# Kernel tuning notes

Measured on AMD Instinct MI355X. Metric: run time of the kernel, lower is better.

The kernel has to match this reference:

```python
import jax, jax.numpy as jnp
import numpy as np

MARGIN = 0.3  # from init_kwargs
N, D = 4096, 128


def _pairwise_sqdist(a, b):
    # ||a_i - b_j||^2 via the matmul identity; avoids an [N, N, D] intermediate.
    a2 = jnp.sum(a * a, axis=1)[:, None]
    b2 = jnp.sum(b * b, axis=1)[None, :]
    return a2 + b2 - 2.0 * (a @ b.T)


def setup_inputs() -> dict:
    key = jax.random.key(0)
    k1, k2 = jax.random.split(key)
    pair1 = jax.random.normal(k1, (N, D), dtype=jnp.float32)
    pair2 = jax.random.normal(k2, (N, D), dtype=jnp.float32)
    return {"pair1": pair1, "pair2": pair2}


def reference(pair1, pair2):
    n = pair1.shape[0]
    # positive distance per anchor: ||pair1[i] - pair2[i]||^2
    dist_ap = jnp.sum((pair1 - pair2) ** 2, axis=1)  # [N]
    D1 = _pairwise_sqdist(pair1, pair1)  # dist_an1[i, j]
    D2 = _pairwise_sqdist(pair1, pair2)  # dist_an2[i, j]
    L1 = jax.nn.relu(dist_ap[:, None] - D1 + MARGIN)  # [N, N]
    L2 = jax.nn.relu(dist_ap[:, None] - D2 + MARGIN)  # [N, N]
    # exclude j == i (the original `continue`); relu outputs are >= 0 and the
    # original hard-mining max starts at 0.0, so zeroing the diagonal is exact.
    offdiag = 1.0 - jnp.eye(n, dtype=L1.dtype)
    L1m = L1 * offdiag
    L2m = L2 * offdiag
    # online hard example mining: max loss per anchor over all 2*(N-1) negatives
    sub_loss = jnp.mean(jnp.maximum(jnp.max(L1m, axis=1), jnp.max(L2m, axis=1)))
    # average over all counted triplets: cnt = 2 * N * (N - 1)
    all_loss = (jnp.sum(L1m) + jnp.sum(L2m)) / (2.0 * n * (n - 1))
    return (sub_loss, all_loss)
```

## Files before the change

### kernel.cpp

```cpp
#include <hip/hip_runtime.h>
#include <hip/hip_bf16.h>

#define NN 4096
#define DD 128
#define MARGIN_F 0.3f
#define JC 128
#define GX (NN / JC)
#define GY (NN / 128)
#define NBLOCKS (GX * GY)
#define NT (JC / 16)

typedef __attribute__((ext_vector_type(8))) short bf16x8;
typedef __attribute__((ext_vector_type(4))) float f32x4;
typedef __attribute__((ext_vector_type(2))) float f32x2;


__device__ __forceinline__ ushort f2bf(float f) {
  __hip_bfloat16 h = __float2bfloat16(f);
  return *reinterpret_cast<ushort*>(&h);
}

__global__ __launch_bounds__(256) void ptl_prep(
    const float* __restrict__ p1, const float* __restrict__ p2,
    ushort* __restrict__ p1t, ushort* __restrict__ p2t,
    float* __restrict__ a2, float* __restrict__ b2, float* __restrict__ c,
    unsigned int* __restrict__ rowmax, float* __restrict__ sumacc,
    unsigned int* __restrict__ donecnt) {
  int row = blockIdx.x * 4 + (threadIdx.x >> 6);
  int lane = threadIdx.x & 63;
  float2 x = ((const float2*)(p1 + (size_t)row * DD))[lane];
  float2 y = ((const float2*)(p2 + (size_t)row * DD))[lane];
  ushort2 xb, yb;
  xb.x = f2bf(x.x); xb.y = f2bf(x.y);
  yb.x = f2bf(y.x); yb.y = f2bf(y.y);
  int k = lane * 2;
  size_t idx = (size_t)(row >> 4) * 2048 + (size_t)(k >> 5) * 512 +
               (size_t)((k & 31) >> 3) * 128 + (size_t)(row & 15) * 8 +
               (size_t)(k & 7);
  *(ushort2*)(p1t + idx) = xb;
  *(ushort2*)(p2t + idx) = yb;

  float sa = x.x * x.x + x.y * x.y;
  float sb = y.x * y.x + y.y * y.y;
  float d0 = x.x - y.x, d1 = x.y - y.y;
  float sd = d0 * d0 + d1 * d1;
#pragma unroll
  for (int off = 32; off > 0; off >>= 1) {
    sa += __shfl_down(sa, off);
    sb += __shfl_down(sb, off);
    sd += __shfl_down(sd, off);
  }
  if (lane == 0) {
    a2[row] = sa;
    b2[row] = sb;
    c[row] = sd - sa + MARGIN_F;
    rowmax[row] = 0u;
  }
  if (blockIdx.x == 0 && threadIdx.x == 0) {
    *sumacc = 0.f;
    *donecnt = 0u;
  }
}

__global__ __launch_bounds__(256) void ptl_mfma(
    const ushort* __restrict__ p1t, const ushort* __restrict__ p2t,
    const float* __restrict__ a2v, const float* __restrict__ b2v,
    const float* __restrict__ cvv, unsigned int* __restrict__ rowmax,
    float* __restrict__ sumacc, unsigned int* __restrict__ donecnt,
    float* __restrict__ out) {
  const int tid = threadIdx.x;
  const int w = tid >> 6;
  const int lane = tid & 63;
  const int col16 = lane & 15;
  const int quad = lane >> 4;
  const int rowBase = (blockIdx.y * 4 + w) * 32;
  const int jBase = blockIdx.x * JC;
  const int lofs = quad * 128 + col16 * 8;

  __shared__ float wsum[4];
  __shared__ float wm[4];
  __shared__ unsigned int ticket;

  bf16x8 afr[2][4];
#pragma unroll
  for (int st = 0; st < 2; ++st) {
    const ushort* pa = p1t + ((size_t)(rowBase >> 4) + st) * 2048 + lofs;
#pragma unroll
    for (int s = 0; s < 4; ++s) afr[st][s] = *(const bf16x8*)(pa + s * 512);
  }

  float cv[2][4];
#pragma unroll
  for (int st = 0; st < 2; ++st)
#pragma unroll
    for (int r = 0; r < 4; ++r) cv[st][r] = cvv[rowBase + st * 16 + quad * 4 + r];

  const ushort* pb1 = p1t + (size_t)(jBase >> 4) * 2048 + lofs;
  const ushort* pb2 = p2t + (size_t)(jBase >> 4) * 2048 + lofs;

  f32x2 lsum2 = {0.f, 0.f};
  f32x2 rmax2[2][4];
#pragma unroll
  for (int st = 0; st < 2; ++st)
#pragma unroll
    for (int r = 0; r < 4; ++r) rmax2[st][r] = (f32x2){0.f, 0.f};

#pragma unroll
  for (int jt = 0; jt < NT; ++jt) {
    bf16x8 b1[4], b2[4];
#pragma unroll
    for (int s = 0; s < 4; ++s) {
      b1[s] = *(const bf16x8*)(pb1 + (size_t)jt * 2048 + s * 512);
      b2[s] = *(const bf16x8*)(pb2 + (size_t)jt * 2048 + s * 512);
    }
    f32x4 acc[2][2];
#pragma unroll
    for (int st = 0; st < 2; ++st)
#pragma unroll
      for (int m = 0; m < 2; ++m) acc[st][m] = (f32x4){0.f, 0.f, 0.f, 0.f};
#pragma unroll
    for (int s = 0; s < 4; ++s) {
      acc[0][0] = __builtin_amdgcn_mfma_f32_16x16x32_bf16(afr[0][s], b1[s], acc[0][0], 0, 0, 0);
      acc[1][0] = __builtin_amdgcn_mfma_f32_16x16x32_bf16(afr[1][s], b1[s], acc[1][0], 0, 0, 0);
      acc[0][1] = __builtin_amdgcn_mfma_f32_16x16x32_bf16(afr[0][s], b2[s], acc[0][1], 0, 0, 0);
      acc[1][1] = __builtin_amdgcn_mfma_f32_16x16x32_bf16(afr[1][s], b2[s], acc[1][1], 0, 0, 0);
    }

    const int jcol = jBase + jt * 16 + col16;
    f32x2 nj = { a2v[jcol], b2v[jcol] };
#pragma unroll
    for (int st = 0; st < 2; ++st) {
      const bool diagT = (jBase + jt * 16) == (rowBase + st * 16);
#pragma unroll
      for (int r = 0; r < 4; ++r) {
        f32x2 t = { acc[st][0][r], acc[st][1][r] };
        f32x2 v = t * 2.f + (cv[st][r] - nj);
        v.x = fmaxf(v.x, 0.f);
        v.y = fmaxf(v.y, 0.f);
        if (diagT && col16 == quad * 4 + r) v = (f32x2){0.f, 0.f};
        lsum2 += v;
        rmax2[st][r].x = fmaxf(rmax2[st][r].x, v.x);
        rmax2[st][r].y = fmaxf(rmax2[st][r].y, v.y);
      }
    }
  }

  float lsum = lsum2.x + lsum2.y;
  float rmax[2][4];
#pragma unroll
  for (int st = 0; st < 2; ++st)
#pragma unroll
    for (int r = 0; r < 4; ++r)
      rmax[st][r] = fmaxf(rmax2[st][r].x, rmax2[st][r].y);

#pragma unroll
  for (int off = 8; off > 0; off >>= 1)
#pragma unroll
    for (int st = 0; st < 2; ++st)
#pragma unroll
      for (int r = 0; r < 4; ++r)
        rmax[st][r] = fmaxf(rmax[st][r], __shfl_xor(rmax[st][r], off));
  if (col16 == 0) {
#pragma unroll
    for (int st = 0; st < 2; ++st)
#pragma unroll
      for (int r = 0; r < 4; ++r)
        atomicMax(&rowmax[rowBase + st * 16 + quad * 4 + r],
                  __float_as_uint(rmax[st][r]));
  }

#pragma unroll
  for (int off = 32; off > 0; off >>= 1) lsum += __shfl_down(lsum, off);
  if (lane == 0) wsum[w] = lsum;
  __syncthreads();
  if (tid == 0) {
    atomicAdd(sumacc, wsum[0] + wsum[1] + wsum[2] + wsum[3]);
    __threadfence();
    ticket = atomicAdd(donecnt, 1u);
  }
  __syncthreads();

  if (ticket == NBLOCKS - 1) {
    __threadfence();
    float sm = 0.f;
#pragma unroll 4
    for (int i = tid; i < NN; i += 256)
      sm += __uint_as_float(atomicMax(&rowmax[i], 0u));
#pragma unroll
    for (int off = 32; off > 0; off >>= 1) sm += __shfl_down(sm, off);
    if (lane == 0) wm[w] = sm;
    __syncthreads();
    if (tid == 0) {
      float total = atomicAdd(sumacc, 0.f);
      out[0] = (wm[0] + wm[1] + wm[2] + wm[3]) / (float)NN;
      out[1] = total / (2.0f * (float)NN * (float)(NN - 1));
    }
  }
}

extern "C" void kernel_launch(void* const* d_in, const int* in_sizes, int n_in,
                              void* d_out, int out_size, void* d_ws, size_t ws_size,
                              hipStream_t stream) {
  const float* p1 = (const float*)d_in[0];
  const float* p2 = (const float*)d_in[1];
  ushort* p1t = (ushort*)d_ws;
  ushort* p2t = p1t + (size_t)NN * DD;
  float* a2 = (float*)(p2t + (size_t)NN * DD);
  float* b2 = a2 + NN;
  float* c = b2 + NN;
  unsigned int* rowmax = (unsigned int*)(c + NN);
  float* sumacc = (float*)(rowmax + NN);
  unsigned int* donecnt = (unsigned int*)(sumacc + 1);

  ptl_prep<<<NN / 4, 256, 0, stream>>>(p1, p2, p1t, p2t, a2, b2, c,
                                       rowmax, sumacc, donecnt);

  dim3 grid(GX, GY);
  ptl_mfma<<<grid, 256, 0, stream>>>(p1t, p2t, a2, b2, c, rowmax, sumacc,
                                     donecnt, (float*)d_out);
}
```

Before: 98.19 us.

## Stage B tiles in LDS with double-buffered direct loads; split sum atomics

Within a block, the four waves now share the column (B) bf16 tiles. Each wave's share is loaded into a double-buffered LDS array with global_load_lds and read back from LDS for the MFMAs, replacing four redundant per-wave global loads. The single global sum accumulator is split into 16 partial slots picked by block id, and the last block reduces them. This cuts global/L2 traffic and atomic contention, at the cost of a barrier every tile step and a reliance on correct wait handling for the direct-to-LDS loads.

```diff
diff --git a/kernel.cpp b/kernel.cpp
--- a/kernel.cpp
+++ b/kernel.cpp
@@ -20,11 +20,17 @@
   return *reinterpret_cast<ushort*>(&h);
 }
 
+__device__ __forceinline__ void gload_lds16(const ushort* g, ushort* l) {
+  __builtin_amdgcn_global_load_lds(
+      (const __attribute__((address_space(1))) void*)g,
+      (__attribute__((address_space(3))) void*)l, 16, 0, 0);
+}
+
 __global__ __launch_bounds__(256) void ptl_prep(
     const float* __restrict__ p1, const float* __restrict__ p2,
     ushort* __restrict__ p1t, ushort* __restrict__ p2t,
     float* __restrict__ a2, float* __restrict__ b2, float* __restrict__ c,
-    unsigned int* __restrict__ rowmax, float* __restrict__ sumacc,
+    unsigned int* __restrict__ rowmax, float* __restrict__ sumpart,
     unsigned int* __restrict__ donecnt) {
   int row = blockIdx.x * 4 + (threadIdx.x >> 6);
   int lane = threadIdx.x & 63;
@@ -56,9 +62,9 @@
     c[row] = sd - sa + MARGIN_F;
     rowmax[row] = 0u;
   }
-  if (blockIdx.x == 0 && threadIdx.x == 0) {
-    *sumacc = 0.f;
-    *donecnt = 0u;
+  if (blockIdx.x == 0) {
+    if (threadIdx.x < 16) sumpart[threadIdx.x] = 0.f;
+    if (threadIdx.x == 16) *donecnt = 0u;
   }
 }
 
@@ -66,21 +72,32 @@
     const ushort* __restrict__ p1t, const ushort* __restrict__ p2t,
     const float* __restrict__ a2v, const float* __restrict__ b2v,
     const float* __restrict__ cvv, unsigned int* __restrict__ rowmax,
-    float* __restrict__ sumacc, unsigned int* __restrict__ donecnt,
+    float* __restrict__ sumpart, unsigned int* __restrict__ donecnt,
     float* __restrict__ out) {
   const int tid = threadIdx.x;
   const int w = tid >> 6;
   const int lane = tid & 63;
   const int col16 = lane & 15;
   const int quad = lane >> 4;
-  const int rowBase = (blockIdx.y * 4 + w) * 32;
+  const int rowBase = blockIdx.y * 128 + w * 32;
   const int jBase = blockIdx.x * JC;
   const int lofs = quad * 128 + col16 * 8;
 
+  __shared__ __align__(16) ushort ldsB[2][2][2048];
   __shared__ float wsum[4];
   __shared__ float wm[4];
   __shared__ unsigned int ticket;
 
+  const int arr = w >> 1;
+  const int half = w & 1;
+  const ushort* gB = (arr ? p2t : p1t) + (size_t)(jBase >> 4) * 2048 +
+                     half * 1024 + lane * 8;
+  ushort* lB0 = &ldsB[0][arr][half * 1024];
+  ushort* lB1 = &ldsB[1][arr][half * 1024];
+
+  gload_lds16(gB, lB0);
+  gload_lds16(gB + 512, lB0 + 512);
+
   bf16x8 afr[2][4];
 #pragma unroll
   for (int st = 0; st < 2; ++st) {
@@ -95,9 +112,6 @@
 #pragma unroll
     for (int r = 0; r < 4; ++r) cv[st][r] = cvv[rowBase + st * 16 + quad * 4 + r];
 
-  const ushort* pb1 = p1t + (size_t)(jBase >> 4) * 2048 + lofs;
-  const ushort* pb2 = p2t + (size_t)(jBase >> 4) * 2048 + lofs;
-
   f32x2 lsum2 = {0.f, 0.f};
   f32x2 rmax2[2][4];
 #pragma unroll
@@ -107,11 +121,20 @@
 
 #pragma unroll
   for (int jt = 0; jt < NT; ++jt) {
+    const int cur = jt & 1;
+    __syncthreads();
+    if (jt + 1 < NT) {
+      const ushort* g = gB + (size_t)(jt + 1) * 2048;
+      ushort* l = cur ? lB0 : lB1;
+      gload_lds16(g, l);
+      gload_lds16(g + 512, l + 512);
+    }
+
     bf16x8 b1[4], b2[4];
 #pragma unroll
     for (int s = 0; s < 4; ++s) {
-      b1[s] = *(const bf16x8*)(pb1 + (size_t)jt * 2048 + s * 512);
-      b2[s] = *(const bf16x8*)(pb2 + (size_t)jt * 2048 + s * 512);
+      b1[s] = *(const bf16x8*)&ldsB[cur][0][s * 512 + lofs];
+      b2[s] = *(const bf16x8*)&ldsB[cur][1][s * 512 + lofs];
     }
     f32x4 acc[2][2];
 #pragma unroll
@@ -173,8 +196,9 @@
   for (int off = 32; off > 0; off >>= 1) lsum += __shfl_down(lsum, off);
   if (lane == 0) wsum[w] = lsum;
   __syncthreads();
+  const int bid = blockIdx.y * GX + blockIdx.x;
   if (tid == 0) {
-    atomicAdd(sumacc, wsum[0] + wsum[1] + wsum[2] + wsum[3]);
+    atomicAdd(&sumpart[bid & 15], wsum[0] + wsum[1] + wsum[2] + wsum[3]);
     __threadfence();
     ticket = atomicAdd(donecnt, 1u);
   }
@@ -189,11 +213,16 @@
 #pragma unroll
     for (int off = 32; off > 0; off >>= 1) sm += __shfl_down(sm, off);
     if (lane == 0) wm[w] = sm;
+    float sp = 0.f;
+    if (w == 0) {
+      sp = (lane < 16) ? atomicAdd(&sumpart[lane], 0.f) : 0.f;
+#pragma unroll
+      for (int off = 8; off > 0; off >>= 1) sp += __shfl_down(sp, off);
+    }
     __syncthreads();
     if (tid == 0) {
-      float total = atomicAdd(sumacc, 0.f);
       out[0] = (wm[0] + wm[1] + wm[2] + wm[3]) / (float)NN;
-      out[1] = total / (2.0f * (float)NN * (float)(NN - 1));
+      out[1] = sp / (2.0f * (float)NN * (float)(NN - 1));
     }
   }
 }
@@ -209,13 +238,13 @@
   float* b2 = a2 + NN;
   float* c = b2 + NN;
   unsigned int* rowmax = (unsigned int*)(c + NN);
-  float* sumacc = (float*)(rowmax + NN);
-  unsigned int* donecnt = (unsigned int*)(sumacc + 1);
+  float* sumpart = (float*)(rowmax + NN);
+  unsigned int* donecnt = (unsigned int*)(sumpart + 16);
 
   ptl_prep<<<NN / 4, 256, 0, stream>>>(p1, p2, p1t, p2t, a2, b2, c,
-                                       rowmax, sumacc, donecnt);
+                                       rowmax, sumpart, donecnt);
 
   dim3 grid(GX, GY);
-  ptl_mfma<<<grid, 256, 0, stream>>>(p1t, p2t, a2, b2, c, rowmax, sumacc,
+  ptl_mfma<<<grid, 256, 0, stream>>>(p1t, p2t, a2, b2, c, rowmax, sumpart,
                                      donecnt, (float*)d_out);
 }
```

Result: faster. 92.84 us (-5.4%).
